# Performance work log

Hardware: AMD Instinct MI355X
Metric: run time of the kernel (lower is better)

The kernel has to match this reference:

```python
import jax, jax.numpy as jnp
import numpy as np


def setup_inputs() -> dict:
    key = jax.random.key(0)
    ks = jax.random.split(key, 6)
    B, C, D, H, O = 4096, 64, 512, 1024, 1
    z = jax.random.normal(ks[0], (B, D), dtype=jnp.float32)
    company_id = jax.random.randint(ks[1], (B,), 0, C)
    # PyTorch Linear default init ~ U(-1/sqrt(fan_in), 1/sqrt(fan_in)); use scaled normals for simplicity
    W1 = jax.random.normal(ks[2], (C, D, H), dtype=jnp.float32) / np.sqrt(D)
    b1 = jax.random.normal(ks[3], (C, H), dtype=jnp.float32) * 0.01
    W2 = jax.random.normal(ks[4], (C, H, O), dtype=jnp.float32) / np.sqrt(H)
    b2 = jax.random.normal(ks[5], (C, O), dtype=jnp.float32) * 0.01
    return {"z": z, "company_id": company_id, "W1": W1, "b1": b1, "W2": W2, "b2": b2}


def reference(z, company_id, W1, b1, W2, b2):
    # Faithful to original: every company head is applied to the full batch,
    # then the single needed row per sample is gathered (dropout is identity in eval).
    # h: [B, C, H]
    h = jnp.einsum("bd,cdh->bch", z, W1) + b1[None, :, :]
    h = jax.nn.gelu(h, approximate=False)  # nn.GELU default = exact erf GELU
    # all_outputs: [B, C, O]
    all_outputs = jnp.einsum("bch,cho->bco", h, W2) + b2[None, :, :]
    # gather the per-sample company row -> [B, O]
    outputs = jnp.take_along_axis(all_outputs, company_id[:, None, None], axis=1)[:, 0, :]
    return outputs
```

## Files before the change

kernel.cpp:

```cpp
#include <hip/hip_runtime.h>

typedef float f32x16 __attribute__((ext_vector_type(16)));
typedef short s16x8  __attribute__((ext_vector_type(8)));

#define B_SZ 4096
#define C_N  64
#define D_K  512
#define H_N  1024
#define BK   16
#define NT   32
#define ROWS 32
#define ZP_OFF_BYTES 32768
#define ZP_ROWS (B_SZ + 128)

__device__ __forceinline__ short f2bf(float f){
  unsigned u = __float_as_uint(f);
  u += 0x7FFFu + ((u >> 16) & 1u);
  return (short)(u >> 16);
}
__device__ __forceinline__ float erf_fast(float x){
  float ax = fabsf(x);
  float t = __builtin_amdgcn_rcpf(1.0f + 0.3275911f * ax);
  float p = t * (0.254829592f + t * (-0.284496736f + t * (1.421413741f +
            t * (-1.453152027f + t * 1.061405429f))));
  float r = 1.0f - p * __expf(-ax * ax);
  return copysignf(r, x);
}
__device__ __forceinline__ float gelu_exact(float x){
  return 0.5f * x * (1.0f + erf_fast(x * 0.70710678118654752f));
}

__global__ void k_prep(const int* __restrict__ cid, const float* __restrict__ b2,
                       int* __restrict__ offsets, int* __restrict__ bucket,
                       float* __restrict__ out){
  __shared__ int hist[C_N];
  const int tid = threadIdx.x;
  if (tid < C_N) hist[tid] = 0;
  __syncthreads();
  for (int i = tid; i < B_SZ; i += 1024) atomicAdd(&hist[cid[i]], 1);
  __syncthreads();
  if (tid < 64){
    int v = hist[tid];
    int x = v;
    #pragma unroll
    for (int d = 1; d < 64; d <<= 1){
      int y = __shfl_up(x, d, 64);
      if (tid >= d) x += y;
    }
    offsets[tid] = x - v;
    if (tid == 63) offsets[64] = x;
    hist[tid] = x - v;
  }
  __syncthreads();
  for (int i = tid; i < B_SZ; i += 1024){
    int c = cid[i];
    int p = atomicAdd(&hist[c], 1);
    bucket[p] = i;
    out[i] = b2[c];
  }
}

__global__ void k_zpack(const float* __restrict__ z, const int* __restrict__ bucket,
                        short* __restrict__ zp){
  int u = blockIdx.x * 256 + threadIdx.x;
  int slot = u >> 6;
  int k0 = (u & 63) * 8;
  const float* src = z + (size_t)bucket[slot] * D_K + k0;
  float4 a = *(const float4*)src;
  float4 b = *(const float4*)(src + 4);
  s16x8 v;
  v[0]=f2bf(a.x); v[1]=f2bf(a.y); v[2]=f2bf(a.z); v[3]=f2bf(a.w);
  v[4]=f2bf(b.x); v[5]=f2bf(b.y); v[6]=f2bf(b.z); v[7]=f2bf(b.w);
  *(s16x8*)(zp + ((size_t)slot << 9) + k0) = v;
}

__global__ __launch_bounds__(256, 4) void k_main(
    const short* __restrict__ zp, const float* __restrict__ W1,
    const float* __restrict__ b1, const float* __restrict__ W2,
    const int* __restrict__ offsets, const int* __restrict__ bucket,
    float* __restrict__ out)
{
  __shared__ s16x8 A_lds[NT * 64];
  __shared__ float B_lds[2][BK * 128];
  __shared__ float partial[ROWS];

  const int bid = blockIdx.x;
  const int c = bid & 63;
  const int o = bid >> 6;
  const int mc = o & 3, hs = o >> 2;
  const int off_c = offsets[c];
  const int n_c = offsets[c + 1] - off_c;
  const int rb = mc * ROWS;
  if (rb >= n_c) return;

  const int tid  = threadIdx.x;
  const int lane = tid & 63, wave = tid >> 6;
  const int l31 = lane & 31, lhi = lane >> 5;
  const int hcol = hs * 128 + wave * 32 + l31;
  const float b1v = b1[c * H_N + hcol];
  const float w2v = W2[c * H_N + hcol];
  const float* Wpanel = W1 + (size_t)c * D_K * H_N + hs * 128;

  if (tid < ROWS) partial[tid] = 0.0f;

  const int r0 = tid >> 5;
  const int hc = (tid & 31) * 4;
  auto stage = [&](int t, int buf){
    const float* src = Wpanel + (size_t)(t * BK + r0) * H_N + hc;
    float* dst = &B_lds[buf][r0 * 128 + hc];
    __builtin_amdgcn_global_load_lds(
      (const __attribute__((address_space(1))) void*)src,
      (__attribute__((address_space(3))) void*)dst, 16, 0, 0);
    __builtin_amdgcn_global_load_lds(
      (const __attribute__((address_space(1))) void*)(src + 8 * H_N),
      (__attribute__((address_space(3))) void*)(dst + 8 * 128), 16, 0, 0);
  };

  stage(0, 0);

  #pragma unroll
  for (int j = 0; j < 8; ++j){
    int u = tid + 256 * j;
    int ks = u >> 6, lu = u & 63;
    int row = lu & 31, lh = lu >> 5;
    A_lds[u] = *(const s16x8*)(zp + ((size_t)(off_c + rb + row) << 9) + ks * BK + lh * 8);
  }
  __syncthreads();

  f32x16 acc = 0;

  for (int t = 0; t < NT; ++t){
    if (t + 1 < NT) stage(t + 1, (t + 1) & 1);
    const float* Bt = &B_lds[t & 1][0];
    s16x8 bf;
    #pragma unroll
    for (int e = 0; e < 8; ++e)
      bf[e] = f2bf(Bt[(lhi * 8 + e) * 128 + wave * 32 + l31]);
    s16x8 af = A_lds[t * 64 + lane];
    acc = __builtin_amdgcn_mfma_f32_32x32x16_bf16(af, bf, acc, 0, 0, 0);
    __syncthreads();
  }

  #pragma unroll
  for (int r = 0; r < 16; ++r){
    int r_loc = (r & 3) + 8 * (r >> 2) + 4 * lhi;
    float s = gelu_exact(acc[r] + b1v) * w2v;
    s += __shfl_xor(s, 1, 64);
    s += __shfl_xor(s, 2, 64);
    s += __shfl_xor(s, 4, 64);
    s += __shfl_xor(s, 8, 64);
    s += __shfl_xor(s, 16, 64);
    if (l31 == 0 && rb + r_loc < n_c)
      atomicAdd(&partial[r_loc], s);
  }
  __syncthreads();
  if (tid < ROWS){
    int g = rb + tid;
    if (g < n_c)
      atomicAdd(&out[bucket[off_c + g]], partial[tid]);
  }
}

extern "C" void kernel_launch(void* const* d_in, const int* in_sizes, int n_in,
                              void* d_out, int out_size, void* d_ws, size_t ws_size,
                              hipStream_t stream){
  const float* z  = (const float*)d_in[0];
  const int*   cid= (const int*)  d_in[1];
  const float* W1 = (const float*)d_in[2];
  const float* b1 = (const float*)d_in[3];
  const float* W2 = (const float*)d_in[4];
  const float* b2 = (const float*)d_in[5];
  float* out = (float*)d_out;

  int*   ws      = (int*)d_ws;
  int*   offsets = ws;
  int*   bucket  = ws + 128;
  short* zp      = (short*)((char*)d_ws + ZP_OFF_BYTES);

  k_prep <<<1, 1024, 0, stream>>>(cid, b2, offsets, bucket, out);
  k_zpack<<<1024, 256, 0, stream>>>(z, bucket, zp);
  k_main <<<C_N * 32, 256, 0, stream>>>(zp, W1, b1, W2, offsets, bucket, out);
}
```

Before: 61.56 us.

## Read each W1 panel once per company and deepen the staging pipeline

Each block now covers every sample row of one company for one 128-column H slice. It loops over 128-row chunks with four MFMA accumulators, instead of separate blocks for each 32-row chunk re-reading the same W1 panel. The grid shrinks to 512 blocks, which cuts redundant fp32 W1 traffic from HBM. A and B tiles are both streamed into LDS with global_load_lds through a 4-buffer ring, using explicit vmcnt waits and raw barriers. The cost is fewer blocks for latency hiding, a larger LDS footprint, and hand-counted waitcnt logic that is fragile if the loads change.

Measured after the change: 52.71 us. 14.4% less time.

```diff
diff --git a/kernel.cpp b/kernel.cpp
--- a/kernel.cpp
+++ b/kernel.cpp
@@ -9,7 +9,7 @@
 #define H_N  1024
 #define BK   16
 #define NT   32
-#define ROWS 32
+#define ROWS 128
 #define ZP_OFF_BYTES 32768
 #define ZP_ROWS (B_SZ + 128)
 
@@ -74,24 +74,21 @@
   *(s16x8*)(zp + ((size_t)slot << 9) + k0) = v;
 }
 
-__global__ __launch_bounds__(256, 4) void k_main(
+__global__ __launch_bounds__(256, 2) void k_main(
     const short* __restrict__ zp, const float* __restrict__ W1,
     const float* __restrict__ b1, const float* __restrict__ W2,
     const int* __restrict__ offsets, const int* __restrict__ bucket,
     float* __restrict__ out)
 {
-  __shared__ s16x8 A_lds[NT * 64];
-  __shared__ float B_lds[2][BK * 128];
+  __shared__ float B_lds[4][BK * 128];
+  __shared__ char  A_lds[4][4096];
   __shared__ float partial[ROWS];
 
   const int bid = blockIdx.x;
-  const int c = bid & 63;
-  const int o = bid >> 6;
-  const int mc = o & 3, hs = o >> 2;
+  const int c = bid & 63, hs = bid >> 6;
   const int off_c = offsets[c];
   const int n_c = offsets[c + 1] - off_c;
-  const int rb = mc * ROWS;
-  if (rb >= n_c) return;
+  if (n_c == 0) return;
 
   const int tid  = threadIdx.x;
   const int lane = tid & 63, wave = tid >> 6;
@@ -101,63 +98,80 @@
   const float w2v = W2[c * H_N + hcol];
   const float* Wpanel = W1 + (size_t)c * D_K * H_N + hs * 128;
 
+  const int r0 = tid >> 5;
+  const int hc = (tid & 31) * 4;
+  const int arow = tid >> 1;
+  const int akh  = (tid & 1) * 8;
+
   if (tid < ROWS) partial[tid] = 0.0f;
 
-  const int r0 = tid >> 5;
-  const int hc = (tid & 31) * 4;
-  auto stage = [&](int t, int buf){
-    const float* src = Wpanel + (size_t)(t * BK + r0) * H_N + hc;
-    float* dst = &B_lds[buf][r0 * 128 + hc];
-    __builtin_amdgcn_global_load_lds(
-      (const __attribute__((address_space(1))) void*)src,
-      (__attribute__((address_space(3))) void*)dst, 16, 0, 0);
-    __builtin_amdgcn_global_load_lds(
-      (const __attribute__((address_space(1))) void*)(src + 8 * H_N),
-      (__attribute__((address_space(3))) void*)(dst + 8 * 128), 16, 0, 0);
-  };
+  for (int rb = 0; rb < n_c; rb += ROWS){
+    const short* zrow = zp + ((size_t)(off_c + rb + arow) << 9) + akh;
 
-  stage(0, 0);
+    auto stage = [&](int t){
+      const int s = t & 3;
+      const float* bsrc = Wpanel + (size_t)(t * BK + r0) * H_N + hc;
+      __builtin_amdgcn_global_load_lds(
+        (const __attribute__((address_space(1))) void*)bsrc,
+        (__attribute__((address_space(3))) void*)(&B_lds[s][r0 * 128 + hc]), 16, 0, 0);
+      __builtin_amdgcn_global_load_lds(
+        (const __attribute__((address_space(1))) void*)(bsrc + 8 * H_N),
+        (__attribute__((address_space(3))) void*)(&B_lds[s][(r0 + 8) * 128 + hc]), 16, 0, 0);
+      __builtin_amdgcn_global_load_lds(
+        (const __attribute__((address_space(1))) void*)(zrow + t * BK),
+        (__attribute__((address_space(3))) void*)(&A_lds[s][tid * 16]), 16, 0, 0);
+    };
 
-  #pragma unroll
-  for (int j = 0; j < 8; ++j){
-    int u = tid + 256 * j;
-    int ks = u >> 6, lu = u & 63;
-    int row = lu & 31, lh = lu >> 5;
-    A_lds[u] = *(const s16x8*)(zp + ((size_t)(off_c + rb + row) << 9) + ks * BK + lh * 8);
-  }
-  __syncthreads();
+    stage(0); stage(1); stage(2);
 
-  f32x16 acc = 0;
+    f32x16 acc[4];
+    acc[0] = 0; acc[1] = 0; acc[2] = 0; acc[3] = 0;
 
-  for (int t = 0; t < NT; ++t){
-    if (t + 1 < NT) stage(t + 1, (t + 1) & 1);
-    const float* Bt = &B_lds[t & 1][0];
-    s16x8 bf;
+    for (int t = 0; t < NT; ++t){
+      if (t + 3 < NT) stage(t + 3);
+      if      (t <  NT - 3) asm volatile("s_waitcnt vmcnt(9)" ::: "memory");
+      else if (t == NT - 3) asm volatile("s_waitcnt vmcnt(6)" ::: "memory");
+      else if (t == NT - 2) asm volatile("s_waitcnt vmcnt(3)" ::: "memory");
+      else                  asm volatile("s_waitcnt vmcnt(0)" ::: "memory");
+      __builtin_amdgcn_s_barrier();
+
+      const int s = t & 3;
+      const float* Bt = &B_lds[s][0];
+      s16x8 bf;
+      #pragma unroll
+      for (int e = 0; e < 8; ++e)
+        bf[e] = f2bf(Bt[(lhi * 8 + e) * 128 + wave * 32 + l31]);
+      const s16x8* At = (const s16x8*)&A_lds[s][0];
+      #pragma unroll
+      for (int m = 0; m < 4; ++m){
+        s16x8 af = At[(m * 32 + l31) * 2 + lhi];
+        acc[m] = __builtin_amdgcn_mfma_f32_32x32x16_bf16(af, bf, acc[m], 0, 0, 0);
+      }
+      __builtin_amdgcn_s_barrier();
+    }
+
     #pragma unroll
-    for (int e = 0; e < 8; ++e)
-      bf[e] = f2bf(Bt[(lhi * 8 + e) * 128 + wave * 32 + l31]);
-    s16x8 af = A_lds[t * 64 + lane];
-    acc = __builtin_amdgcn_mfma_f32_32x32x16_bf16(af, bf, acc, 0, 0, 0);
+    for (int m = 0; m < 4; ++m){
+      #pragma unroll
+      for (int r = 0; r < 16; ++r){
+        int r_loc = m * 32 + (r & 3) + 8 * (r >> 2) + 4 * lhi;
+        float v = gelu_exact(acc[m][r] + b1v) * w2v;
+        v += __shfl_xor(v, 1, 64);
+        v += __shfl_xor(v, 2, 64);
+        v += __shfl_xor(v, 4, 64);
+        v += __shfl_xor(v, 8, 64);
+        v += __shfl_xor(v, 16, 64);
+        if (l31 == 0 && rb + r_loc < n_c)
+          atomicAdd(&partial[r_loc], v);
+      }
+    }
     __syncthreads();
-  }
-
-  #pragma unroll
-  for (int r = 0; r < 16; ++r){
-    int r_loc = (r & 3) + 8 * (r >> 2) + 4 * lhi;
-    float s = gelu_exact(acc[r] + b1v) * w2v;
-    s += __shfl_xor(s, 1, 64);
-    s += __shfl_xor(s, 2, 64);
-    s += __shfl_xor(s, 4, 64);
-    s += __shfl_xor(s, 8, 64);
-    s += __shfl_xor(s, 16, 64);
-    if (l31 == 0 && rb + r_loc < n_c)
-      atomicAdd(&partial[r_loc], s);
-  }
-  __syncthreads();
-  if (tid < ROWS){
-    int g = rb + tid;
-    if (g < n_c)
-      atomicAdd(&out[bucket[off_c + g]], partial[tid]);
+    if (tid < ROWS){
+      int g = rb + tid;
+      if (g < n_c)
+        atomicAdd(&out[bucket[off_c + g]], partial[tid]);
+      partial[tid] = 0.0f;
+    }
   }
 }
 
@@ -179,5 +193,5 @@
 
   k_prep <<<1, 1024, 0, stream>>>(cid, b2, offsets, bucket, out);
   k_zpack<<<1024, 256, 0, stream>>>(z, bucket, zp);
-  k_main <<<C_N * 32, 256, 0, stream>>>(zp, W1, b1, W2, offsets, bucket, out);
+  k_main <<<C_N * 8, 256, 0, stream>>>(zp, W1, b1, W2, offsets, bucket, out);
 }
```
